# Kernel tuning notes

Hardware: AMD Instinct MI355X
Metric: run time of the kernel (lower is better)

The kernel has to match this reference:

```python
import jax, jax.numpy as jnp
import numpy as np

B = 256        # number of graphs (mol rows)
N = 262144     # total residues
H = 128        # hidden_dim


def setup_inputs() -> dict:
    key = jax.random.key(0)
    ks = jax.random.split(key, 8)
    mol = jax.random.normal(ks[0], (B, H), dtype=jnp.float32)
    prot = jax.random.normal(ks[1], (N, H), dtype=jnp.float32)
    batch = jnp.sort(jax.random.randint(ks[2], (N,), 0, B)).astype(jnp.int64)
    s = 1.0 / np.sqrt(H)
    Wq = jax.random.uniform(ks[3], (H, H), jnp.float32, -s, s)
    bq = jax.random.uniform(ks[4], (H,), jnp.float32, -s, s)
    Wk = jax.random.uniform(ks[5], (H, H), jnp.float32, -s, s)
    bk = jax.random.uniform(ks[6], (H,), jnp.float32, -s, s)
    sm = 1.0 / np.sqrt(2 * H)
    Wm = jax.random.uniform(ks[7], (1, 2 * H), jnp.float32, -sm, sm)  # merge, no bias
    return {"mol": mol, "prot": prot, "batch": batch,
            "Wq": Wq, "bq": bq, "Wk": Wk, "bk": bk, "Wm": Wm}


def reference(mol, prot, batch, Wq, bq, Wk, bk, Wm):
    q = jax.nn.relu(mol @ Wq.T + bq)                      # [B, H]
    # repeat_interleave(q, degree(batch)) with sorted batch == gather q[batch]
    r = q[batch]                                          # [N, H]
    k = jax.nn.relu(prot @ Wk.T + bk)                     # [N, H]
    score = jnp.concatenate([k, r], axis=-1) @ Wm.T       # [N, 1]
    # segment softmax over residues of each graph (stable)
    m = jax.ops.segment_max(score, batch, num_segments=B)  # [B, 1]
    e = jnp.exp(score - m[batch])                          # [N, 1]
    denom = jax.ops.segment_sum(e, batch, num_segments=B)  # [B, 1]
    attn = e / denom[batch]                                # [N, 1]
    o = jax.ops.segment_sum(k * attn, batch, num_segments=B)  # [B, H]
    return (o, q)
```

## Files before the change

kernel.cpp:

```cpp
#include <hip/hip_runtime.h>
#include <hip/hip_bf16.h>

#define H    128
#define NB   256
#define NRES 262144

typedef __attribute__((ext_vector_type(4))) float f32x4;
typedef __attribute__((ext_vector_type(8))) short short8;

__device__ __forceinline__ short bf16cvt(float f) {
  unsigned u = __builtin_bit_cast(unsigned, f);
  unsigned r = (u + 0x7fffu + ((u >> 16) & 1u)) >> 16;
  return (short)r;
}

__device__ __forceinline__ short8 pack_bf16x8(f32x4 x, f32x4 y) {
  short8 v;
  v[0] = bf16cvt(x[0]); v[1] = bf16cvt(x[1]);
  v[2] = bf16cvt(x[2]); v[3] = bf16cvt(x[3]);
  v[4] = bf16cvt(y[0]); v[5] = bf16cvt(y[1]);
  v[6] = bf16cvt(y[2]); v[7] = bf16cvt(y[3]);
  return v;
}

__device__ __forceinline__ int lower_bound_i(const int* __restrict__ a, int n, int v) {
  int lo = 0, hi = n;
  while (lo < hi) { int mid = (lo + hi) >> 1; if (a[mid] < v) lo = mid + 1; else hi = mid; }
  return lo;
}

__global__ __launch_bounds__(128) void qkern(
    const float* __restrict__ mol, const float* __restrict__ Wq,
    const float* __restrict__ bq, const float* __restrict__ Wm,
    float* __restrict__ out, float* __restrict__ s2) {
  int b = blockIdx.x, h = threadIdx.x;
  const float* mrow = mol + b * H;
  const float* wrow = Wq + h * H;
  float acc = bq[h];
#pragma unroll 8
  for (int j = 0; j < H; ++j) acc = fmaf(mrow[j], wrow[j], acc);
  float q = fmaxf(acc, 0.f);
  out[NB * H + b * H + h] = q;
  out[b * H + h] = 0.f;
  float p = q * Wm[H + h];
#pragma unroll
  for (int off = 32; off >= 1; off >>= 1) p += __shfl_xor(p, off);
  __shared__ float red[2];
  if ((threadIdx.x & 63) == 0) red[threadIdx.x >> 6] = p;
  __syncthreads();
  if (threadIdx.x == 0) s2[b] = red[0] + red[1];
}

__device__ __forceinline__ void fill_wk_frags(short* __restrict__ bfrag,
                                              const float* __restrict__ Wk, int tid) {
  for (int slot = tid; slot < 32 * 64; slot += 256) {
    int f = slot >> 6, l = slot & 63;
    int ct = f >> 2, kk = f & 3;
    const float* src = Wk + (ct * 16 + (l & 15)) * H + kk * 32 + (l >> 4) * 8;
    f32x4 x = *(const f32x4*)src;
    f32x4 y = *(const f32x4*)(src + 4);
    *(short8*)&bfrag[slot * 8] = pack_bf16x8(x, y);
  }
}

__global__ __launch_bounds__(256) void scorekern(
    const float* __restrict__ prot, const int* __restrict__ batch,
    const float* __restrict__ Wk, const float* __restrict__ bk,
    const float* __restrict__ Wm, const float* __restrict__ s2,
    float* __restrict__ score) {
  __shared__ short bfrag[32 * 64 * 8];
  int tid = threadIdx.x;
  fill_wk_frags(bfrag, Wk, tid);
  __syncthreads();
  int w = tid >> 6, l = tid & 63;
  int cg = l & 15, kg = l >> 4;
  float wm1v[8], bkv[8];
#pragma unroll
  for (int ct = 0; ct < 8; ++ct) { wm1v[ct] = Wm[ct * 16 + cg]; bkv[ct] = bk[ct * 16 + cg]; }
  int gw = blockIdx.x * 4 + w;
  int nw = gridDim.x * 4;
  for (int t = gw; t < NRES / 16; t += nw) {
    int r0 = t * 16;
    const float* pbase = prot + (r0 + cg) * H + kg * 8;
    short8 a[4];
#pragma unroll
    for (int kk = 0; kk < 4; ++kk) {
      f32x4 x = *(const f32x4*)(pbase + kk * 32);
      f32x4 y = *(const f32x4*)(pbase + kk * 32 + 4);
      a[kk] = pack_bf16x8(x, y);
    }
    f32x4 acc[8];
#pragma unroll
    for (int ct = 0; ct < 8; ++ct) acc[ct] = (f32x4){0.f, 0.f, 0.f, 0.f};
#pragma unroll
    for (int ct = 0; ct < 8; ++ct)
#pragma unroll
      for (int kk = 0; kk < 4; ++kk) {
        short8 bf = *(const short8*)&bfrag[((ct * 4 + kk) * 64 + l) * 8];
        acc[ct] = __builtin_amdgcn_mfma_f32_16x16x32_bf16(a[kk], bf, acc[ct], 0, 0, 0);
      }
    float p0 = 0.f, p1 = 0.f, p2 = 0.f, p3 = 0.f;
#pragma unroll
    for (int ct = 0; ct < 8; ++ct) {
      p0 += fmaxf(acc[ct][0] + bkv[ct], 0.f) * wm1v[ct];
      p1 += fmaxf(acc[ct][1] + bkv[ct], 0.f) * wm1v[ct];
      p2 += fmaxf(acc[ct][2] + bkv[ct], 0.f) * wm1v[ct];
      p3 += fmaxf(acc[ct][3] + bkv[ct], 0.f) * wm1v[ct];
    }
#pragma unroll
    for (int off = 1; off < 16; off <<= 1) {
      p0 += __shfl_xor(p0, off); p1 += __shfl_xor(p1, off);
      p2 += __shfl_xor(p2, off); p3 += __shfl_xor(p3, off);
    }
    if (cg < 4) {
      int j = l & 3;
      float pv = (j == 0) ? p0 : (j == 1) ? p1 : (j == 2) ? p2 : p3;
      int n = r0 + kg * 4 + j;
      score[n] = pv + s2[batch[n]];
    }
  }
}

__global__ __launch_bounds__(256) void segred(
    const int* __restrict__ batch, const float* __restrict__ score,
    float* __restrict__ mval, float* __restrict__ dinv) {
  int b = blockIdx.x, tid = threadIdx.x;
  int start = lower_bound_i(batch, NRES, b);
  int end = lower_bound_i(batch, NRES, b + 1);
  float m = -3.0e38f;
  for (int i = start + tid; i < end; i += 256) m = fmaxf(m, score[i]);
#pragma unroll
  for (int off = 32; off >= 1; off >>= 1) m = fmaxf(m, __shfl_xor(m, off));
  __shared__ float red[4];
  if ((tid & 63) == 0) red[tid >> 6] = m;
  __syncthreads();
  m = fmaxf(fmaxf(red[0], red[1]), fmaxf(red[2], red[3]));
  float s = 0.f;
  for (int i = start + tid; i < end; i += 256) s += __expf(score[i] - m);
#pragma unroll
  for (int off = 32; off >= 1; off >>= 1) s += __shfl_xor(s, off);
  __shared__ float red2[4];
  if ((tid & 63) == 0) red2[tid >> 6] = s;
  __syncthreads();
  if (tid == 0) {
    s = red2[0] + red2[1] + red2[2] + red2[3];
    mval[b] = m;
    dinv[b] = (s > 0.f) ? 1.f / s : 0.f;
  }
}

#define SB 8
__global__ __launch_bounds__(256) void outkern(
    const float* __restrict__ prot, const int* __restrict__ batch,
    const float* __restrict__ Wk, const float* __restrict__ bk,
    const float* __restrict__ score, const float* __restrict__ mval,
    const float* __restrict__ dinv, float* __restrict__ out) {
  __shared__ short bfrag[32 * 64 * 8];
  __shared__ float o_sh[H];
  int tid = threadIdx.x;
  int b = blockIdx.x >> 3, sub = blockIdx.x & 7;
  fill_wk_frags(bfrag, Wk, tid);
  if (tid < H) o_sh[tid] = 0.f;
  __syncthreads();
  int start = lower_bound_i(batch, NRES, b);
  int end = lower_bound_i(batch, NRES, b + 1);
  float m = mval[b], inv_d = dinv[b];
  int w = tid >> 6, l = tid & 63;
  int cg = l & 15, kg = l >> 4;
  float bkv[8];
#pragma unroll
  for (int ct = 0; ct < 8; ++ct) bkv[ct] = bk[ct * 16 + cg];
  float op[8] = {0.f, 0.f, 0.f, 0.f, 0.f, 0.f, 0.f, 0.f};
  int ntiles = (end - start + 15) >> 4;
  for (int t = sub * 4 + w; t < ntiles; t += SB * 4) {
    int r0 = start + t * 16;
    int arow = min(r0 + cg, NRES - 1);
    const float* pbase = prot + arow * H + kg * 8;
    short8 a[4];
#pragma unroll
    for (int kk = 0; kk < 4; ++kk) {
      f32x4 x = *(const f32x4*)(pbase + kk * 32);
      f32x4 y = *(const f32x4*)(pbase + kk * 32 + 4);
      a[kk] = pack_bf16x8(x, y);
    }
    f32x4 acc[8];
#pragma unroll
    for (int ct = 0; ct < 8; ++ct) acc[ct] = (f32x4){0.f, 0.f, 0.f, 0.f};
#pragma unroll
    for (int ct = 0; ct < 8; ++ct)
#pragma unroll
      for (int kk = 0; kk < 4; ++kk) {
        short8 bf = *(const short8*)&bfrag[((ct * 4 + kk) * 64 + l) * 8];
        acc[ct] = __builtin_amdgcn_mfma_f32_16x16x32_bf16(a[kk], bf, acc[ct], 0, 0, 0);
      }
    float at0, at1, at2, at3;
    {
      int r = r0 + kg * 4;
      at0 = (r + 0 < end) ? __expf(score[r + 0] - m) * inv_d : 0.f;
      at1 = (r + 1 < end) ? __expf(score[r + 1] - m) * inv_d : 0.f;
      at2 = (r + 2 < end) ? __expf(score[r + 2] - m) * inv_d : 0.f;
      at3 = (r + 3 < end) ? __expf(score[r + 3] - m) * inv_d : 0.f;
    }
#pragma unroll
    for (int ct = 0; ct < 8; ++ct) {
      op[ct] += at0 * fmaxf(acc[ct][0] + bkv[ct], 0.f);
      op[ct] += at1 * fmaxf(acc[ct][1] + bkv[ct], 0.f);
      op[ct] += at2 * fmaxf(acc[ct][2] + bkv[ct], 0.f);
      op[ct] += at3 * fmaxf(acc[ct][3] + bkv[ct], 0.f);
    }
  }
#pragma unroll
  for (int ct = 0; ct < 8; ++ct) {
    op[ct] += __shfl_xor(op[ct], 16);
    op[ct] += __shfl_xor(op[ct], 32);
  }
  if (l < 16) {
#pragma unroll
    for (int ct = 0; ct < 8; ++ct) atomicAdd(&o_sh[ct * 16 + l], op[ct]);
  }
  __syncthreads();
  if (tid < H) atomicAdd(&out[b * H + tid], o_sh[tid]);
}

extern "C" void kernel_launch(void* const* d_in, const int* in_sizes, int n_in,
                              void* d_out, int out_size, void* d_ws, size_t ws_size,
                              hipStream_t stream) {
  const float* mol   = (const float*)d_in[0];
  const float* prot  = (const float*)d_in[1];
  const int*   batch = (const int*)d_in[2];
  const float* Wq    = (const float*)d_in[3];
  const float* bq    = (const float*)d_in[4];
  const float* Wk    = (const float*)d_in[5];
  const float* bk    = (const float*)d_in[6];
  const float* Wm    = (const float*)d_in[7];
  float* out = (float*)d_out;

  float* score = (float*)d_ws;
  float* s2    = score + NRES;
  float* mval  = s2 + NB;
  float* dinv  = mval + NB;

  hipLaunchKernelGGL(qkern, dim3(NB), dim3(128), 0, stream, mol, Wq, bq, Wm, out, s2);
  hipLaunchKernelGGL(scorekern, dim3(2048), dim3(256), 0, stream, prot, batch, Wk, bk, Wm, s2, score);
  hipLaunchKernelGGL(segred, dim3(NB), dim3(256), 0, stream, batch, score, mval, dinv);
  hipLaunchKernelGGL(outkern, dim3(NB * SB), dim3(256), 0, stream, prot, batch, Wk, bk, score, mval, dinv, out);
}
```

Before: 299.5 us.

## Fuse score, segment softmax and weighted sum into one chunked pass

Replaces the separate score, segment-reduce and output kernels with a single chunk kernel. It computes k once per 128-row chunk, keeps it in LDS as bf16, and emits per-graph partial (max, sum, weighted vector) records. A small combine kernel then merges them with an online-softmax rescale. This removes the second read and second matmul over the protein features, and the mol-side score term is dropped because it cancels within a segment. Wk is pre-packed to bf16 once in a prep kernel. The risks are slot aliasing if a graph spans more than 64 chunks and bf16 rounding of k in the weighted sum.

```diff
diff --git a/kernel.cpp b/kernel.cpp
--- a/kernel.cpp
+++ b/kernel.cpp
@@ -1,9 +1,13 @@
 #include <hip/hip_runtime.h>
 #include <hip/hip_bf16.h>
 
-#define H    128
-#define NB   256
-#define NRES 262144
+#define H      128
+#define NB     256
+#define NRES   262144
+#define CHUNK  128
+#define NCHUNK (NRES / CHUNK)
+#define PIECES 64
+#define REC    136
 
 typedef __attribute__((ext_vector_type(4))) float f32x4;
 typedef __attribute__((ext_vector_type(8))) short short8;
@@ -12,6 +16,11 @@
   unsigned u = __builtin_bit_cast(unsigned, f);
   unsigned r = (u + 0x7fffu + ((u >> 16) & 1u)) >> 16;
   return (short)r;
+}
+
+__device__ __forceinline__ float bf16tof(unsigned short u) {
+  unsigned v = ((unsigned)u) << 16;
+  return __builtin_bit_cast(float, v);
 }
 
 __device__ __forceinline__ short8 pack_bf16x8(f32x4 x, f32x4 y) {
@@ -29,59 +38,61 @@
   return lo;
 }
 
-__global__ __launch_bounds__(128) void qkern(
+__global__ __launch_bounds__(256) void prep(
     const float* __restrict__ mol, const float* __restrict__ Wq,
-    const float* __restrict__ bq, const float* __restrict__ Wm,
-    float* __restrict__ out, float* __restrict__ s2) {
-  int b = blockIdx.x, h = threadIdx.x;
-  const float* mrow = mol + b * H;
-  const float* wrow = Wq + h * H;
-  float acc = bq[h];
+    const float* __restrict__ bq, const float* __restrict__ Wk,
+    float* __restrict__ out, short* __restrict__ wkp) {
+  int bid = blockIdx.x, tid = threadIdx.x;
+  if (bid < NB) {
+    if (tid < H) {
+      const float* mrow = mol + bid * H;
+      const float* wrow = Wq + tid * H;
+      float acc = bq[tid];
 #pragma unroll 8
-  for (int j = 0; j < H; ++j) acc = fmaf(mrow[j], wrow[j], acc);
-  float q = fmaxf(acc, 0.f);
-  out[NB * H + b * H + h] = q;
-  out[b * H + h] = 0.f;
-  float p = q * Wm[H + h];
-#pragma unroll
-  for (int off = 32; off >= 1; off >>= 1) p += __shfl_xor(p, off);
-  __shared__ float red[2];
-  if ((threadIdx.x & 63) == 0) red[threadIdx.x >> 6] = p;
-  __syncthreads();
-  if (threadIdx.x == 0) s2[b] = red[0] + red[1];
-}
-
-__device__ __forceinline__ void fill_wk_frags(short* __restrict__ bfrag,
-                                              const float* __restrict__ Wk, int tid) {
-  for (int slot = tid; slot < 32 * 64; slot += 256) {
+      for (int j = 0; j < H; ++j) acc = fmaf(mrow[j], wrow[j], acc);
+      out[NB * H + bid * H + tid] = fmaxf(acc, 0.f);
+    }
+  } else {
+    int slot = (bid - NB) * 256 + tid;
     int f = slot >> 6, l = slot & 63;
     int ct = f >> 2, kk = f & 3;
     const float* src = Wk + (ct * 16 + (l & 15)) * H + kk * 32 + (l >> 4) * 8;
     f32x4 x = *(const f32x4*)src;
     f32x4 y = *(const f32x4*)(src + 4);
-    *(short8*)&bfrag[slot * 8] = pack_bf16x8(x, y);
-  }
-}
-
-__global__ __launch_bounds__(256) void scorekern(
+    *(short8*)&wkp[slot * 8] = pack_bf16x8(x, y);
+  }
+}
+
+__global__ __launch_bounds__(256) void chunkkern(
     const float* __restrict__ prot, const int* __restrict__ batch,
-    const float* __restrict__ Wk, const float* __restrict__ bk,
-    const float* __restrict__ Wm, const float* __restrict__ s2,
-    float* __restrict__ score) {
-  __shared__ short bfrag[32 * 64 * 8];
+    const short* __restrict__ wkp, const float* __restrict__ bk,
+    const float* __restrict__ Wm, float* __restrict__ part) {
+  __shared__ short bfrag[2048 * 8];
+  __shared__ unsigned short k_sh[CHUNK * 132];
+  __shared__ float score_sh[CHUNK];
+  __shared__ float e_sh[CHUNK];
+  __shared__ float vhalf[H];
+  __shared__ int   batch_sh[CHUNK];
+  __shared__ float red[4], red2[4];
+
   int tid = threadIdx.x;
-  fill_wk_frags(bfrag, Wk, tid);
+  int c0row = blockIdx.x * CHUNK;
+
+  for (int i = tid; i < 2048; i += 256)
+    *(short8*)&bfrag[i * 8] = *(const short8*)&wkp[i * 8];
+  if (tid < CHUNK) batch_sh[tid] = batch[c0row + tid];
   __syncthreads();
+
   int w = tid >> 6, l = tid & 63;
   int cg = l & 15, kg = l >> 4;
   float wm1v[8], bkv[8];
 #pragma unroll
   for (int ct = 0; ct < 8; ++ct) { wm1v[ct] = Wm[ct * 16 + cg]; bkv[ct] = bk[ct * 16 + cg]; }
-  int gw = blockIdx.x * 4 + w;
-  int nw = gridDim.x * 4;
-  for (int t = gw; t < NRES / 16; t += nw) {
-    int r0 = t * 16;
-    const float* pbase = prot + (r0 + cg) * H + kg * 8;
+
+#pragma unroll
+  for (int tile = 0; tile < 2; ++tile) {
+    int rbase = w * 32 + tile * 16;
+    const float* pbase = prot + (c0row + rbase + cg) * H + kg * 8;
     short8 a[4];
 #pragma unroll
     for (int kk = 0; kk < 4; ++kk) {
@@ -100,12 +111,20 @@
         acc[ct] = __builtin_amdgcn_mfma_f32_16x16x32_bf16(a[kk], bf, acc[ct], 0, 0, 0);
       }
     float p0 = 0.f, p1 = 0.f, p2 = 0.f, p3 = 0.f;
+    int row0 = rbase + kg * 4;
 #pragma unroll
     for (int ct = 0; ct < 8; ++ct) {
-      p0 += fmaxf(acc[ct][0] + bkv[ct], 0.f) * wm1v[ct];
-      p1 += fmaxf(acc[ct][1] + bkv[ct], 0.f) * wm1v[ct];
-      p2 += fmaxf(acc[ct][2] + bkv[ct], 0.f) * wm1v[ct];
-      p3 += fmaxf(acc[ct][3] + bkv[ct], 0.f) * wm1v[ct];
+      float v0 = fmaxf(acc[ct][0] + bkv[ct], 0.f);
+      float v1 = fmaxf(acc[ct][1] + bkv[ct], 0.f);
+      float v2 = fmaxf(acc[ct][2] + bkv[ct], 0.f);
+      float v3 = fmaxf(acc[ct][3] + bkv[ct], 0.f);
+      p0 += v0 * wm1v[ct]; p1 += v1 * wm1v[ct];
+      p2 += v2 * wm1v[ct]; p3 += v3 * wm1v[ct];
+      int colb = ct * 16 + cg;
+      k_sh[(row0 + 0) * 132 + colb] = (unsigned short)bf16cvt(v0);
+      k_sh[(row0 + 1) * 132 + colb] = (unsigned short)bf16cvt(v1);
+      k_sh[(row0 + 2) * 132 + colb] = (unsigned short)bf16cvt(v2);
+      k_sh[(row0 + 3) * 132 + colb] = (unsigned short)bf16cvt(v3);
     }
 #pragma unroll
     for (int off = 1; off < 16; off <<= 1) {
@@ -115,111 +134,65 @@
     if (cg < 4) {
       int j = l & 3;
       float pv = (j == 0) ? p0 : (j == 1) ? p1 : (j == 2) ? p2 : p3;
-      int n = r0 + kg * 4 + j;
-      score[n] = pv + s2[batch[n]];
-    }
-  }
-}
-
-__global__ __launch_bounds__(256) void segred(
-    const int* __restrict__ batch, const float* __restrict__ score,
-    float* __restrict__ mval, float* __restrict__ dinv) {
-  int b = blockIdx.x, tid = threadIdx.x;
+      score_sh[rbase + kg * 4 + j] = pv;
+    }
+  }
+  __syncthreads();
+
+  int b0 = batch_sh[0], b1 = batch_sh[CHUNK - 1];
+  int slot = blockIdx.x & (PIECES - 1);
+  for (int b = b0; b <= b1; ++b) {
+    int lo, hi;
+    { int L = 0, R = CHUNK; while (L < R) { int M = (L + R) >> 1; if (batch_sh[M] < b) L = M + 1; else R = M; } lo = L; }
+    { int L = 0, R = CHUNK; while (L < R) { int M = (L + R) >> 1; if (batch_sh[M] <= b) L = M + 1; else R = M; } hi = L; }
+    if (hi > lo) {
+      float x = (tid < CHUNK && tid >= lo && tid < hi) ? score_sh[tid] : -3.0e38f;
+#pragma unroll
+      for (int off = 32; off >= 1; off >>= 1) x = fmaxf(x, __shfl_xor(x, off));
+      if (l == 0) red[w] = x;
+      __syncthreads();
+      float m_loc = fmaxf(fmaxf(red[0], red[1]), fmaxf(red[2], red[3]));
+      float e = 0.f;
+      if (tid < CHUNK && tid >= lo && tid < hi) { e = __expf(score_sh[tid] - m_loc); e_sh[tid] = e; }
+      float s = e;
+#pragma unroll
+      for (int off = 32; off >= 1; off >>= 1) s += __shfl_xor(s, off);
+      if (l == 0) red2[w] = s;
+      __syncthreads();
+      float s_loc = red2[0] + red2[1] + red2[2] + red2[3];
+      int c = tid & 127, half = tid >> 7;
+      float acc = 0.f;
+      for (int r = lo + half; r < hi; r += 2)
+        acc += e_sh[r] * bf16tof(k_sh[r * 132 + c]);
+      if (half) vhalf[c] = acc;
+      __syncthreads();
+      float* pp = part + ((size_t)b * PIECES + slot) * REC;
+      if (!half) pp[8 + c] = acc + vhalf[c];
+      if (tid == 0) { pp[0] = m_loc; pp[1] = s_loc; }
+      __syncthreads();
+    }
+  }
+}
+
+__global__ __launch_bounds__(128) void combine(
+    const int* __restrict__ batch, const float* __restrict__ part,
+    float* __restrict__ out) {
+  int b = blockIdx.x, c = threadIdx.x;
   int start = lower_bound_i(batch, NRES, b);
   int end = lower_bound_i(batch, NRES, b + 1);
+  if (end <= start) { out[b * H + c] = 0.f; return; }
+  int c0 = start >> 7, c1 = (end - 1) >> 7;
   float m = -3.0e38f;
-  for (int i = start + tid; i < end; i += 256) m = fmaxf(m, score[i]);
-#pragma unroll
-  for (int off = 32; off >= 1; off >>= 1) m = fmaxf(m, __shfl_xor(m, off));
-  __shared__ float red[4];
-  if ((tid & 63) == 0) red[tid >> 6] = m;
-  __syncthreads();
-  m = fmaxf(fmaxf(red[0], red[1]), fmaxf(red[2], red[3]));
-  float s = 0.f;
-  for (int i = start + tid; i < end; i += 256) s += __expf(score[i] - m);
-#pragma unroll
-  for (int off = 32; off >= 1; off >>= 1) s += __shfl_xor(s, off);
-  __shared__ float red2[4];
-  if ((tid & 63) == 0) red2[tid >> 6] = s;
-  __syncthreads();
-  if (tid == 0) {
-    s = red2[0] + red2[1] + red2[2] + red2[3];
-    mval[b] = m;
-    dinv[b] = (s > 0.f) ? 1.f / s : 0.f;
-  }
-}
-
-#define SB 8
-__global__ __launch_bounds__(256) void outkern(
-    const float* __restrict__ prot, const int* __restrict__ batch,
-    const float* __restrict__ Wk, const float* __restrict__ bk,
-    const float* __restrict__ score, const float* __restrict__ mval,
-    const float* __restrict__ dinv, float* __restrict__ out) {
-  __shared__ short bfrag[32 * 64 * 8];
-  __shared__ float o_sh[H];
-  int tid = threadIdx.x;
-  int b = blockIdx.x >> 3, sub = blockIdx.x & 7;
-  fill_wk_frags(bfrag, Wk, tid);
-  if (tid < H) o_sh[tid] = 0.f;
-  __syncthreads();
-  int start = lower_bound_i(batch, NRES, b);
-  int end = lower_bound_i(batch, NRES, b + 1);
-  float m = mval[b], inv_d = dinv[b];
-  int w = tid >> 6, l = tid & 63;
-  int cg = l & 15, kg = l >> 4;
-  float bkv[8];
-#pragma unroll
-  for (int ct = 0; ct < 8; ++ct) bkv[ct] = bk[ct * 16 + cg];
-  float op[8] = {0.f, 0.f, 0.f, 0.f, 0.f, 0.f, 0.f, 0.f};
-  int ntiles = (end - start + 15) >> 4;
-  for (int t = sub * 4 + w; t < ntiles; t += SB * 4) {
-    int r0 = start + t * 16;
-    int arow = min(r0 + cg, NRES - 1);
-    const float* pbase = prot + arow * H + kg * 8;
-    short8 a[4];
-#pragma unroll
-    for (int kk = 0; kk < 4; ++kk) {
-      f32x4 x = *(const f32x4*)(pbase + kk * 32);
-      f32x4 y = *(const f32x4*)(pbase + kk * 32 + 4);
-      a[kk] = pack_bf16x8(x, y);
-    }
-    f32x4 acc[8];
-#pragma unroll
-    for (int ct = 0; ct < 8; ++ct) acc[ct] = (f32x4){0.f, 0.f, 0.f, 0.f};
-#pragma unroll
-    for (int ct = 0; ct < 8; ++ct)
-#pragma unroll
-      for (int kk = 0; kk < 4; ++kk) {
-        short8 bf = *(const short8*)&bfrag[((ct * 4 + kk) * 64 + l) * 8];
-        acc[ct] = __builtin_amdgcn_mfma_f32_16x16x32_bf16(a[kk], bf, acc[ct], 0, 0, 0);
-      }
-    float at0, at1, at2, at3;
-    {
-      int r = r0 + kg * 4;
-      at0 = (r + 0 < end) ? __expf(score[r + 0] - m) * inv_d : 0.f;
-      at1 = (r + 1 < end) ? __expf(score[r + 1] - m) * inv_d : 0.f;
-      at2 = (r + 2 < end) ? __expf(score[r + 2] - m) * inv_d : 0.f;
-      at3 = (r + 3 < end) ? __expf(score[r + 3] - m) * inv_d : 0.f;
-    }
-#pragma unroll
-    for (int ct = 0; ct < 8; ++ct) {
-      op[ct] += at0 * fmaxf(acc[ct][0] + bkv[ct], 0.f);
-      op[ct] += at1 * fmaxf(acc[ct][1] + bkv[ct], 0.f);
-      op[ct] += at2 * fmaxf(acc[ct][2] + bkv[ct], 0.f);
-      op[ct] += at3 * fmaxf(acc[ct][3] + bkv[ct], 0.f);
-    }
-  }
-#pragma unroll
-  for (int ct = 0; ct < 8; ++ct) {
-    op[ct] += __shfl_xor(op[ct], 16);
-    op[ct] += __shfl_xor(op[ct], 32);
-  }
-  if (l < 16) {
-#pragma unroll
-    for (int ct = 0; ct < 8; ++ct) atomicAdd(&o_sh[ct * 16 + l], op[ct]);
-  }
-  __syncthreads();
-  if (tid < H) atomicAdd(&out[b * H + tid], o_sh[tid]);
+  for (int ch = c0; ch <= c1; ++ch)
+    m = fmaxf(m, part[((size_t)b * PIECES + (ch & (PIECES - 1))) * REC]);
+  float denom = 0.f, v = 0.f;
+  for (int ch = c0; ch <= c1; ++ch) {
+    const float* pp = part + ((size_t)b * PIECES + (ch & (PIECES - 1))) * REC;
+    float wgt = __expf(pp[0] - m);
+    denom += pp[1] * wgt;
+    v += pp[8 + c] * wgt;
+  }
+  out[b * H + c] = (denom > 0.f) ? v / denom : 0.f;
 }
 
 extern "C" void kernel_launch(void* const* d_in, const int* in_sizes, int n_in,
@@ -235,13 +208,10 @@
   const float* Wm    = (const float*)d_in[7];
   float* out = (float*)d_out;
 
-  float* score = (float*)d_ws;
-  float* s2    = score + NRES;
-  float* mval  = s2 + NB;
-  float* dinv  = mval + NB;
-
-  hipLaunchKernelGGL(qkern, dim3(NB), dim3(128), 0, stream, mol, Wq, bq, Wm, out, s2);
-  hipLaunchKernelGGL(scorekern, dim3(2048), dim3(256), 0, stream, prot, batch, Wk, bk, Wm, s2, score);
-  hipLaunchKernelGGL(segred, dim3(NB), dim3(256), 0, stream, batch, score, mval, dinv);
-  hipLaunchKernelGGL(outkern, dim3(NB * SB), dim3(256), 0, stream, prot, batch, Wk, bk, score, mval, dinv, out);
-}
+  short* wkp  = (short*)d_ws;
+  float* part = (float*)((char*)d_ws + 32768);
+
+  hipLaunchKernelGGL(prep, dim3(NB + 8), dim3(256), 0, stream, mol, Wq, bq, Wk, out, wkp);
+  hipLaunchKernelGGL(chunkkern, dim3(NCHUNK), dim3(256), 0, stream, prot, batch, wkp, bk, Wm, part);
+  hipLaunchKernelGGL(combine, dim3(NB), dim3(128), 0, stream, batch, part, out);
+}
```

Result: faster. 242.8 us (-18.9%).
